# Kernel optimization log

Measured on AMD Instinct MI355X. Metric: run time of the kernel, lower is better.

## Reference

```python
import jax, jax.numpy as jnp
import numpy as np

DIM = 2048
N_HEADS = 32
N_KV_HEADS = 4
HEAD_DIM = DIM // N_HEADS  # 64


def _rope_tables(T, head_dim, dtype):
    inv_freq = 1.0 / (10000.0 ** (jnp.arange(0, head_dim, 2, dtype=jnp.float32) / head_dim))
    t = jnp.arange(T, dtype=jnp.float32)
    freqs = jnp.einsum('i,j->ij', t, inv_freq)           # [T, head_dim/2]
    emb = jnp.concatenate([freqs, freqs], axis=-1)        # [T, head_dim]
    return jnp.cos(emb).astype(dtype), jnp.sin(emb).astype(dtype)


def _rotate_half(x):
    d = x.shape[-1] // 2
    return jnp.concatenate([-x[..., d:], x[..., :d]], axis=-1)


def setup_inputs() -> dict:
    key = jax.random.key(0)
    kx, kq, kk, kv, ko = jax.random.split(key, 5)
    s = 1.0 / np.sqrt(DIM)
    return {
        'x': jax.random.normal(kx, (2, 2048, DIM), dtype=jnp.float32),
        'wq': jax.random.normal(kq, (DIM, DIM), dtype=jnp.float32) * s,
        'wk': jax.random.normal(kk, (DIM, DIM // 8), dtype=jnp.float32) * s,
        'wv': jax.random.normal(kv, (DIM, DIM // 8), dtype=jnp.float32) * s,
        'wo': jax.random.normal(ko, (DIM, DIM), dtype=jnp.float32) * s,
    }


def reference(x, wq, wk, wv, wo):
    B, T, C = x.shape
    q = (x @ wq).reshape(B, T, N_HEADS, HEAD_DIM).transpose(0, 2, 1, 3)      # [B,H,T,D]
    k = (x @ wk).reshape(B, T, N_KV_HEADS, HEAD_DIM).transpose(0, 2, 1, 3)   # [B,Hkv,T,D]
    v = (x @ wv).reshape(B, T, N_KV_HEADS, HEAD_DIM).transpose(0, 2, 1, 3)

    cos, sin = _rope_tables(T, HEAD_DIM, x.dtype)  # [T,D]
    q = q * cos + _rotate_half(q) * sin
    k = k * cos + _rotate_half(k) * sin

    rep = N_HEADS // N_KV_HEADS
    k = jnp.repeat(k, rep, axis=1)  # [B,H,T,D]
    v = jnp.repeat(v, rep, axis=1)

    scale = 1.0 / np.sqrt(HEAD_DIM)
    scores = jnp.einsum('bhqd,bhkd->bhqk', q, k) * scale
    causal = jnp.tril(jnp.ones((T, T), dtype=bool))
    scores = jnp.where(causal, scores, jnp.finfo(scores.dtype).min)
    attn = jax.nn.softmax(scores, axis=-1)
    out = jnp.einsum('bhqk,bhkd->bhqd', attn, v)
    out = out.transpose(0, 2, 1, 3).reshape(B, T, C)
    return out @ wo
```

## Files before the change

kernel.cpp:

```cpp
#include <hip/hip_runtime.h>
#include <hip/hip_bf16.h>
#include <stdint.h>

#define DIM 2048
#define TSEQ 2048
#define BATCH 2
#define NH 32
#define NKV 4
#define HD 64
#define MROWS (BATCH*TSEQ)
#define NQKV 2560

typedef __attribute__((ext_vector_type(4))) float f32x4;
typedef __attribute__((ext_vector_type(8))) __bf16 bf16x8;
typedef unsigned short ushort_t;

#define GLDS16(g, l) __builtin_amdgcn_global_load_lds( \
    (const __attribute__((address_space(1))) void*)(g), \
    (__attribute__((address_space(3))) void*)(l), 16, 0, 0)

__device__ __forceinline__ float bflo2f(unsigned int w) {
  union { unsigned int i; float f; } c; c.i = w << 16; return c.f;
}
__device__ __forceinline__ unsigned short f2bf(float f) {
  union { float f; unsigned int i; } c; c.f = f;
  unsigned int x = c.i;
  x += 0x7fffu + ((x >> 16) & 1u);
  return (unsigned short)(x >> 16);
}
__device__ __forceinline__ unsigned short f2bf_fast(float f) {
  union { float f; unsigned int i; } c; c.f = f;
  return (unsigned short)((c.i + 0x8000u) >> 16);
}

__global__ void cast_bf16_k(const float* __restrict__ in, ushort_t* __restrict__ out, int n4) {
  const int i = blockIdx.x * 256 + threadIdx.x;
  if (i >= n4) return;
  const float4 v = ((const float4*)in)[i];
  uint2 p;
  p.x = (unsigned int)f2bf(v.x) | ((unsigned int)f2bf(v.y) << 16);
  p.y = (unsigned int)f2bf(v.z) | ((unsigned int)f2bf(v.w) << 16);
  ((uint2*)out)[i] = p;
}

__global__ void transpose_cast(const float* __restrict__ w, ushort_t* __restrict__ wt, int K, int N) {
  __shared__ float tile[32][33];
  const int bk = blockIdx.x * 32;
  const int bn = blockIdx.y * 32;
  const int tx = threadIdx.x & 31;
  const int ty = threadIdx.x >> 5;
#pragma unroll
  for (int p = 0; p < 4; p++) {
    const int r = ty + p * 8;
    tile[r][tx] = w[(long)(bk + r) * N + bn + tx];
  }
  __syncthreads();
#pragma unroll
  for (int p = 0; p < 4; p++) {
    const int r = ty + p * 8;
    wt[(long)(bn + r) * K + bk + tx] = f2bf(tile[tx][r]);
  }
}

template<int EPI>
__global__ __launch_bounds__(256, 2) void gemm_bt(
    const ushort_t* __restrict__ A, const ushort_t* __restrict__ BT,
    int M, int N, int K,
    float* __restrict__ Cf, ushort_t* __restrict__ Cq,
    ushort_t* __restrict__ Ck, ushort_t* __restrict__ Cv)
{
  __shared__ __align__(16) ushort_t As[128][64];
  __shared__ __align__(16) ushort_t Bs[128][64];
  const int tid  = threadIdx.x;
  const int lane = tid & 63;
  const int wid  = tid >> 6;
  const int wm   = wid >> 1, wn = wid & 1;
  const int l8   = lane >> 3;
  const int c8   = (lane & 7) * 8;
  const long abase = (long)blockIdx.x * 128 * K;
  const long bbase = (long)blockIdx.y * 128 * K;
  const int rsel = lane & 15;
  const int koff = (lane >> 4) * 8;
  f32x4 acc[4][4] = {};

  for (int k0 = 0; k0 < K; k0 += 64) {
    __syncthreads();
#pragma unroll
    for (int i = 0; i < 4; i++) {
      const int r0 = wid * 32 + i * 8;
      GLDS16(&A [abase + (long)(r0 + l8) * K + k0 + c8], &As[r0][0]);
      GLDS16(&BT[bbase + (long)(r0 + l8) * K + k0 + c8], &Bs[r0][0]);
    }
    __syncthreads();
#pragma unroll
    for (int kk = 0; kk < 64; kk += 32) {
      bf16x8 af[4], bfr[4];
#pragma unroll
      for (int m = 0; m < 4; m++) af[m]  = *(const bf16x8*)(&As[wm*64 + m*16 + rsel][kk + koff]);
#pragma unroll
      for (int n = 0; n < 4; n++) bfr[n] = *(const bf16x8*)(&Bs[wn*64 + n*16 + rsel][kk + koff]);
#pragma unroll
      for (int m = 0; m < 4; m++)
#pragma unroll
        for (int n = 0; n < 4; n++)
          acc[m][n] = __builtin_amdgcn_mfma_f32_16x16x32_bf16(af[m], bfr[n], acc[m][n], 0, 0, 0);
    }
  }

  const int rbase = blockIdx.x * 128 + wm * 64 + (lane >> 4) * 4;
  const int cbase = blockIdx.y * 128 + wn * 64 + (lane & 15);
#pragma unroll
  for (int m = 0; m < 4; m++) {
#pragma unroll
    for (int n = 0; n < 4; n++) {
      const int gn = cbase + n * 16;
#pragma unroll
      for (int j = 0; j < 4; j++) {
        const int gm = rbase + m * 16 + j;
        const float v = acc[m][n][j];
        if (EPI == 1) {
          Cf[(long)gm * N + gn] = v;
        } else {
          if (gn < DIM) {
            Cq[(long)gm * DIM + gn] = f2bf(v);
          } else {
            const int x = gn - DIM;
            const int hkv = (x >> 6) & 3;
            const int d = x & 63;
            const int b = gm >> 11;
            const int t = gm & (TSEQ - 1);
            if (x < 256) Ck[((long)(b * NKV + hkv) * TSEQ + t) * HD + d] = f2bf(v);
            else         Cv[((long)(b * NKV + hkv) * HD + d) * TSEQ + t] = f2bf(v);
          }
        }
      }
    }
  }
}

#define LOG1E4_D32 0.2878231366242557f
#define QSCALE 0.1803368801111243f

__global__ void rope_q_k(ushort_t* __restrict__ q) {
  const int idx = blockIdx.x * 256 + threadIdx.x;
  const int m  = idx >> 10;
  const int rr = idx & 1023;
  const int h  = rr >> 5;
  const int d  = rr & 31;
  const int t  = m & (TSEQ - 1);
  const float ang = (float)t * __expf(-(float)d * LOG1E4_D32);
  float s_, c_;
  __sincosf(ang, &s_, &c_);
  const long base = (long)m * DIM + h * 64 + d;
  const float q0 = bflo2f(q[base]);
  const float q1 = bflo2f(q[base + 32]);
  q[base]      = f2bf((q0 * c_ - q1 * s_) * QSCALE);
  q[base + 32] = f2bf((q1 * c_ + q0 * s_) * QSCALE);
}

__global__ void rope_k_k(ushort_t* __restrict__ k) {
  const int idx = blockIdx.x * 256 + threadIdx.x;
  const int row = idx >> 5;
  const int d   = idx & 31;
  const int t   = row & (TSEQ - 1);
  const float ang = (float)t * __expf(-(float)d * LOG1E4_D32);
  float s_, c_;
  __sincosf(ang, &s_, &c_);
  const long base = (long)row * HD + d;
  const float k0 = bflo2f(k[base]);
  const float k1 = bflo2f(k[base + 32]);
  k[base]      = f2bf(k0 * c_ - k1 * s_);
  k[base + 32] = f2bf(k1 * c_ + k0 * s_);
}

__global__ __launch_bounds__(512, 4) void attn_mfma(
    const ushort_t* __restrict__ q, const ushort_t* __restrict__ k,
    const ushort_t* __restrict__ vt, ushort_t* __restrict__ o)
{
  __shared__ __align__(16) ushort_t Ks[64][72];
  __shared__ __align__(16) ushort_t Vs[64][72];
  __shared__ __align__(16) ushort_t Ps[8][16][72];

  const int tid  = threadIdx.x;
  const int lane = tid & 63;
  const int wid  = tid >> 6;
  const int l15  = lane & 15;
  const int lg   = lane >> 4;

  const int bh  = blockIdx.x & 63;
  const int qt  = (TSEQ / 128 - 1) - (blockIdx.x >> 6);
  const int h   = bh & (NH - 1);
  const int b   = bh >> 5;
  const int hkv = h >> 3;
  const int qbase = qt * 128;
  const int qw0   = qbase + wid * 16;

  bf16x8 qf[2];
  {
    const ushort_t* qp = q + ((long)(b * TSEQ) + qw0 + l15) * DIM + h * 64 + lg * 8;
    qf[0] = *(const bf16x8*)(qp);
    qf[1] = *(const bf16x8*)(qp + 32);
  }

  const ushort_t* kb_ = k  + (long)(b * NKV + hkv) * TSEQ * HD;
  const ushort_t* vb_ = vt + (long)(b * NKV + hkv) * HD * TSEQ;

  float m_g = -1e30f;
  float l_c = 0.f;
  f32x4 o_[4] = {};

  const int srow = tid >> 3;
  const int sc   = (tid & 7) * 8;

  const int nkv = 2 * (qt + 1);

  *(uint4*)(&Ks[srow][sc]) = *(const uint4*)(&kb_[(long)srow * HD + sc]);
  *(uint4*)(&Vs[srow][sc]) = *(const uint4*)(&vb_[(long)srow * TSEQ + sc]);
  __syncthreads();

  for (int kbv = 0; kbv < nkv; kbv++) {
    const int kb0 = kbv * 64;
    const bool pf = (kbv + 1 < nkv);
    uint4 kr = {}, vr = {};
    if (pf) {
      kr = *(const uint4*)(&kb_[(long)(kb0 + 64 + srow) * HD + sc]);
      vr = *(const uint4*)(&vb_[(long)srow * TSEQ + kb0 + 64 + sc]);
    }

    if (kb0 <= qw0 + 15) {
      f32x4 st[4] = {};
#pragma unroll
      for (int kt = 0; kt < 4; kt++) {
#pragma unroll
        for (int c = 0; c < 2; c++) {
          const bf16x8 kf = *(const bf16x8*)(&Ks[kt * 16 + l15][c * 32 + lg * 8]);
          st[kt] = __builtin_amdgcn_mfma_f32_16x16x32_bf16(kf, qf[c], st[kt], 0, 0, 0);
        }
      }

      if (kb0 + 63 > qw0) {
        const int qg = qw0 + l15;
#pragma unroll
        for (int kt = 0; kt < 4; kt++) {
          const int kg0 = kb0 + kt * 16 + lg * 4;
#pragma unroll
          for (int j = 0; j < 4; j++) {
            if (kg0 + j > qg) st[kt][j] = -1e30f;
          }
        }
      }

      float pm;
      {
        float mk0 = fmaxf(fmaxf(st[0][0], st[0][1]), fmaxf(st[0][2], st[0][3]));
        float mk1 = fmaxf(fmaxf(st[1][0], st[1][1]), fmaxf(st[1][2], st[1][3]));
        float mk2 = fmaxf(fmaxf(st[2][0], st[2][1]), fmaxf(st[2][2], st[2][3]));
        float mk3 = fmaxf(fmaxf(st[3][0], st[3][1]), fmaxf(st[3][2], st[3][3]));
        pm = fmaxf(fmaxf(mk0, mk1), fmaxf(mk2, mk3));
      }
      pm = fmaxf(pm, __shfl_xor(pm, 16, 64));
      pm = fmaxf(pm, __shfl_xor(pm, 32, 64));

      if (__any(pm > m_g + 8.f)) {
        const float mnew = fmaxf(m_g, pm);
        const float alc  = exp2f(m_g - mnew);
        m_g = mnew;
        l_c *= alc;
        float alr[4];
#pragma unroll
        for (int j = 0; j < 4; j++)
          alr[j] = __shfl(alc, (lane & 48) | (lg * 4 + j), 64);
#pragma unroll
        for (int nt = 0; nt < 4; nt++)
#pragma unroll
          for (int j = 0; j < 4; j++) o_[nt][j] *= alr[j];
      }

      float rs = 0.f;
#pragma unroll
      for (int kt = 0; kt < 4; kt++) {
        const float p0 = exp2f(st[kt][0] - m_g);
        const float p1 = exp2f(st[kt][1] - m_g);
        const float p2 = exp2f(st[kt][2] - m_g);
        const float p3 = exp2f(st[kt][3] - m_g);
        rs += (p0 + p1) + (p2 + p3);
        unsigned int d0, d1;
        asm("v_cvt_pk_bf16_f32 %0, %1, %2" : "=v"(d0) : "v"(p0), "v"(p1));
        asm("v_cvt_pk_bf16_f32 %0, %1, %2" : "=v"(d1) : "v"(p2), "v"(p3));
        *(unsigned int*)(&Ps[wid][l15][kt * 16 + lg * 4])     = d0;
        *(unsigned int*)(&Ps[wid][l15][kt * 16 + lg * 4 + 2]) = d1;
      }
      rs += __shfl_xor(rs, 16, 64);
      rs += __shfl_xor(rs, 32, 64);
      l_c += rs;

#pragma unroll
      for (int c = 0; c < 2; c++) {
        const bf16x8 pa = *(const bf16x8*)(&Ps[wid][l15][c * 32 + lg * 8]);
#pragma unroll
        for (int nt = 0; nt < 4; nt++) {
          const bf16x8 vf = *(const bf16x8*)(&Vs[nt * 16 + l15][c * 32 + lg * 8]);
          o_[nt] = __builtin_amdgcn_mfma_f32_16x16x32_bf16(pa, vf, o_[nt], 0, 0, 0);
        }
      }
    }

    __syncthreads();
    if (pf) {
      *(uint4*)(&Ks[srow][sc]) = kr;
      *(uint4*)(&Vs[srow][sc]) = vr;
    }
    __syncthreads();
  }

  const long orow = (long)(b * TSEQ) + qw0;
#pragma unroll
  for (int j = 0; j < 4; j++) {
    const float inv = 1.f / __shfl(l_c, (lane & 48) | (lg * 4 + j), 64);
#pragma unroll
    for (int nt = 0; nt < 4; nt++)
      o[(orow + lg * 4 + j) * DIM + h * 64 + nt * 16 + l15] = f2bf_fast(o_[nt][j] * inv);
  }
}

extern "C" void kernel_launch(void* const* d_in, const int* in_sizes, int n_in,
                              void* d_out, int out_size, void* d_ws, size_t ws_size,
                              hipStream_t stream) {
  const float* x  = (const float*)d_in[0];
  const float* wq = (const float*)d_in[1];
  const float* wk = (const float*)d_in[2];
  const float* wv = (const float*)d_in[3];
  const float* wo = (const float*)d_in[4];
  float* out = (float*)d_out;

  ushort_t* ws = (ushort_t*)d_ws;
  const long NXB = (long)MROWS * DIM;
  ushort_t* xb   = ws;
  ushort_t* wtq  = xb  + NXB;
  ushort_t* woT  = wtq + (long)NQKV * DIM;
  ushort_t* qws  = woT + (long)DIM * DIM;
  ushort_t* kws  = qws + NXB;
  ushort_t* vtws = kws + (long)BATCH * NKV * TSEQ * HD;
  ushort_t* aws  = vtws + (long)BATCH * NKV * TSEQ * HD;

  cast_bf16_k<<<(int)(NXB / 1024), 256, 0, stream>>>(x, xb, (int)(NXB / 4));
  transpose_cast<<<dim3(64, 64), 256, 0, stream>>>(wq, wtq, DIM, DIM);
  transpose_cast<<<dim3(64, 8),  256, 0, stream>>>(wk, wtq + (long)DIM  * DIM, DIM, 256);
  transpose_cast<<<dim3(64, 8),  256, 0, stream>>>(wv, wtq + (long)2304 * DIM, DIM, 256);
  transpose_cast<<<dim3(64, 64), 256, 0, stream>>>(wo, woT, DIM, DIM);

  gemm_bt<0><<<dim3(32, 20), 256, 0, stream>>>(xb, wtq, MROWS, NQKV, DIM,
                                               nullptr, qws, kws, vtws);
  rope_q_k<<<(MROWS * NH * 32) / 256, 256, 0, stream>>>(qws);
  rope_k_k<<<(BATCH * NKV * TSEQ * 32) / 256, 256, 0, stream>>>(kws);

  attn_mfma<<<BATCH * NH * (TSEQ / 128), 512, 0, stream>>>(qws, kws, vtws, aws);

  gemm_bt<1><<<dim3(32, 16), 256, 0, stream>>>(aws, woT, MROWS, DIM, DIM,
                                               out, nullptr, nullptr, nullptr);
}
```

Baseline: 237.0 us.

## Double-buffer K/V tiles with XOR-swizzled LDS and a single barrier per step

Attention K/V shared tiles become double-buffered, so the next tile is written into the alternate buffer and only one barrier per iteration is needed instead of two. Row padding is removed and replaced by an XOR swizzle of 8-element column groups for K, V and P to avoid LDS bank conflicts while shrinking LDS. Launch bounds rise to 6 blocks per CU to exploit the smaller footprint. This risks extra register pressure from the higher occupancy target and relies on a hand-written waitcnt and barrier being correct.

```diff
diff --git a/kernel.cpp b/kernel.cpp
--- a/kernel.cpp
+++ b/kernel.cpp
@@ -173,19 +173,20 @@
   k[base + 32] = f2bf(k1 * c_ + k0 * s_);
 }
 
-__global__ __launch_bounds__(512, 4) void attn_mfma(
+__global__ __launch_bounds__(512, 6) void attn_mfma(
     const ushort_t* __restrict__ q, const ushort_t* __restrict__ k,
     const ushort_t* __restrict__ vt, ushort_t* __restrict__ o)
 {
-  __shared__ __align__(16) ushort_t Ks[64][72];
-  __shared__ __align__(16) ushort_t Vs[64][72];
-  __shared__ __align__(16) ushort_t Ps[8][16][72];
+  __shared__ __align__(16) ushort_t Ks[2][64][64];
+  __shared__ __align__(16) ushort_t Vs[2][64][64];
+  __shared__ __align__(16) ushort_t Ps[8][16][64];
 
   const int tid  = threadIdx.x;
   const int lane = tid & 63;
   const int wid  = tid >> 6;
   const int l15  = lane & 15;
   const int lg   = lane >> 4;
+  const int sw   = l15 & 7;
 
   const int bh  = blockIdx.x & 63;
   const int qt  = (TSEQ / 128 - 1) - (blockIdx.x >> 6);
@@ -210,22 +211,24 @@
   f32x4 o_[4] = {};
 
   const int srow = tid >> 3;
-  const int sc   = (tid & 7) * 8;
+  const int sgc  = (tid & 7) * 8;
+  const int slc  = (((tid & 7) ^ (srow & 7))) * 8;
 
   const int nkv = 2 * (qt + 1);
 
-  *(uint4*)(&Ks[srow][sc]) = *(const uint4*)(&kb_[(long)srow * HD + sc]);
-  *(uint4*)(&Vs[srow][sc]) = *(const uint4*)(&vb_[(long)srow * TSEQ + sc]);
-  __syncthreads();
+  *(uint4*)(&Ks[0][srow][slc]) = *(const uint4*)(&kb_[(long)srow * HD + sgc]);
+  *(uint4*)(&Vs[0][srow][slc]) = *(const uint4*)(&vb_[(long)srow * TSEQ + sgc]);
+  int cur = 0;
 
   for (int kbv = 0; kbv < nkv; kbv++) {
     const int kb0 = kbv * 64;
     const bool pf = (kbv + 1 < nkv);
     uint4 kr = {}, vr = {};
     if (pf) {
-      kr = *(const uint4*)(&kb_[(long)(kb0 + 64 + srow) * HD + sc]);
-      vr = *(const uint4*)(&vb_[(long)srow * TSEQ + kb0 + 64 + sc]);
-    }
+      kr = *(const uint4*)(&kb_[(long)(kb0 + 64 + srow) * HD + sgc]);
+      vr = *(const uint4*)(&vb_[(long)srow * TSEQ + kb0 + 64 + sgc]);
+    }
+    asm volatile("s_waitcnt lgkmcnt(0)\n\ts_barrier" ::: "memory");
 
     if (kb0 <= qw0 + 15) {
       f32x4 st[4] = {};
@@ -233,7 +236,7 @@
       for (int kt = 0; kt < 4; kt++) {
 #pragma unroll
         for (int c = 0; c < 2; c++) {
-          const bf16x8 kf = *(const bf16x8*)(&Ks[kt * 16 + l15][c * 32 + lg * 8]);
+          const bf16x8 kf = *(const bf16x8*)(&Ks[cur][kt * 16 + l15][((4*c + lg) ^ sw) * 8]);
           st[kt] = __builtin_amdgcn_mfma_f32_16x16x32_bf16(kf, qf[c], st[kt], 0, 0, 0);
         }
       }
@@ -287,8 +290,9 @@
         unsigned int d0, d1;
         asm("v_cvt_pk_bf16_f32 %0, %1, %2" : "=v"(d0) : "v"(p0), "v"(p1));
         asm("v_cvt_pk_bf16_f32 %0, %1, %2" : "=v"(d1) : "v"(p2), "v"(p3));
-        *(unsigned int*)(&Ps[wid][l15][kt * 16 + lg * 4])     = d0;
-        *(unsigned int*)(&Ps[wid][l15][kt * 16 + lg * 4 + 2]) = d1;
+        const int g0 = ((2 * kt + (lg >> 1)) ^ sw) * 8 + (lg & 1) * 4;
+        *(unsigned int*)(&Ps[wid][l15][g0])     = d0;
+        *(unsigned int*)(&Ps[wid][l15][g0 + 2]) = d1;
       }
       rs += __shfl_xor(rs, 16, 64);
       rs += __shfl_xor(rs, 32, 64);
@@ -296,21 +300,20 @@
 
 #pragma unroll
       for (int c = 0; c < 2; c++) {
-        const bf16x8 pa = *(const bf16x8*)(&Ps[wid][l15][c * 32 + lg * 8]);
+        const bf16x8 pa = *(const bf16x8*)(&Ps[wid][l15][((4*c + lg) ^ sw) * 8]);
 #pragma unroll
         for (int nt = 0; nt < 4; nt++) {
-          const bf16x8 vf = *(const bf16x8*)(&Vs[nt * 16 + l15][c * 32 + lg * 8]);
+          const bf16x8 vf = *(const bf16x8*)(&Vs[cur][nt * 16 + l15][((4*c + lg) ^ sw) * 8]);
           o_[nt] = __builtin_amdgcn_mfma_f32_16x16x32_bf16(pa, vf, o_[nt], 0, 0, 0);
         }
       }
     }
 
-    __syncthreads();
     if (pf) {
-      *(uint4*)(&Ks[srow][sc]) = kr;
-      *(uint4*)(&Vs[srow][sc]) = vr;
-    }
-    __syncthreads();
+      *(uint4*)(&Ks[cur ^ 1][srow][slc]) = kr;
+      *(uint4*)(&Vs[cur ^ 1][srow][slc]) = vr;
+    }
+    cur ^= 1;
   }
 
   const long orow = (long)(b * TSEQ) + qw0;
```

New measurement: 226.7 us. 1.05x faster.
